# Kernel tuning notes

Measured on AMD Instinct MI355X. Metric: run time of the kernel, lower is better.

The kernel has to match this reference:

```python
import jax, jax.numpy as jnp
import numpy as np

D_MODEL = 1024
N_HEADS = 16
HEAD_DIM = 64
D_FF = 4096


def rmsnorm(x, w):
    eps = jnp.finfo(x.dtype).eps
    var = jnp.mean(jnp.square(x), axis=-1, keepdims=True)
    return x * jax.lax.rsqrt(var + eps) * w


def setup_inputs() -> dict:
    key = jax.random.key(0)
    ks = jax.random.split(key, 8)
    d, h, hd, dff = D_MODEL, N_HEADS, HEAD_DIM, D_FF
    s = 0.02
    return {
        "x": jax.random.normal(ks[0], (2, 2048, d), dtype=jnp.float32),
        "norm_w": jnp.ones((d,), dtype=jnp.float32),
        "Wq": jax.random.normal(ks[1], (d, h * hd), dtype=jnp.float32) * s,
        "Wk": jax.random.normal(ks[2], (d, h * hd), dtype=jnp.float32) * s,
        "Wv": jax.random.normal(ks[3], (d, h * hd), dtype=jnp.float32) * s,
        "Wo": jax.random.normal(ks[4], (h * hd, d), dtype=jnp.float32) * s,
        "W1": jax.random.normal(ks[5], (d, dff), dtype=jnp.float32) * s,
        "W2": jax.random.normal(ks[6], (dff, d), dtype=jnp.float32) * s,
    }


def reference(x, norm_w, Wq, Wk, Wv, Wo, W1, W2):
    B, T, d = x.shape
    h, hd = N_HEADS, HEAD_DIM
    scale = 1.0 / np.sqrt(hd)

    xn = rmsnorm(x, norm_w)

    # attention branch
    q = (xn @ Wq).reshape(B, T, h, hd).transpose(0, 2, 1, 3)  # [B,h,T,hd]
    k = (xn @ Wk).reshape(B, T, h, hd).transpose(0, 2, 1, 3)
    v = (xn @ Wv).reshape(B, T, h, hd).transpose(0, 2, 1, 3)
    attn = jnp.einsum("bhqd,bhkd->bhqk", q, k) * scale
    causal = jnp.tril(jnp.ones((T, T), dtype=bool))
    attn = jnp.where(causal, attn, -jnp.inf)
    attn = jax.nn.softmax(attn, axis=-1)
    out = jnp.einsum("bhqk,bhkd->bhqd", attn, v)
    out = out.transpose(0, 2, 1, 3).reshape(B, T, h * hd)
    attn_out = out @ Wo

    # FFN branch
    ffn_out = jax.nn.silu(xn @ W1) @ W2

    return x + attn_out + ffn_out
```

## Files before the change

kernel.cpp:

```cpp
#include <hip/hip_runtime.h>

#define DM   1024
#define DFF  4096
#define NH   16
#define HD   64
#define TT   2048
#define BT   4096
#define KC   5120

typedef unsigned short u16;
typedef unsigned int   u32;
typedef __attribute__((ext_vector_type(8))) short s16x8;
typedef __attribute__((ext_vector_type(4))) float f32x4;

__device__ __forceinline__ u16 f2bf(float f) {
  u32 u = __builtin_bit_cast(u32, f);
  u += 0x7fffu + ((u >> 16) & 1u);
  return (u16)(u >> 16);
}

__device__ __forceinline__ void gl2lds16(const void* g, void* l) {
  __builtin_amdgcn_global_load_lds((__attribute__((address_space(1))) void*)(g),
                                   (__attribute__((address_space(3))) void*)(l),
                                   16, 0, 0);
}

#define S_BARRIER() do { __builtin_amdgcn_s_barrier(); __builtin_amdgcn_sched_barrier(0); } while (0)
#define VMWAIT(n)   asm volatile("s_waitcnt vmcnt(" #n ")" ::: "memory")

__global__ __launch_bounds__(256) void rmsnorm_k(const float* __restrict__ x,
                                                 const float* __restrict__ w,
                                                 u16* __restrict__ xn) {
  const int row = blockIdx.x;
  const int t = threadIdx.x;
  const float4 v = ((const float4*)(x + (size_t)row * DM))[t];
  float ss = v.x*v.x + v.y*v.y + v.z*v.z + v.w*v.w;
  #pragma unroll
  for (int off = 32; off; off >>= 1) ss += __shfl_xor(ss, off, 64);
  __shared__ float red[4];
  if ((t & 63) == 0) red[t >> 6] = ss;
  __syncthreads();
  const float tot = red[0] + red[1] + red[2] + red[3];
  const float r = __builtin_amdgcn_rsqf(tot * (1.0f / DM) + 1.1920929e-7f);
  const float4 wv = ((const float4*)w)[t];
  u16* o = xn + (size_t)row * DM + t * 4;
  o[0] = f2bf(v.x * r * wv.x);
  o[1] = f2bf(v.y * r * wv.y);
  o[2] = f2bf(v.z * r * wv.z);
  o[3] = f2bf(v.w * r * wv.w);
}

__global__ __launch_bounds__(256) void wtrans_k(const float* __restrict__ W,
                                                u16* __restrict__ Wt,
                                                int K, int N, int pitch, int koff) {
  __shared__ float tile[32][33];
  const int n0 = blockIdx.x * 32, k0 = blockIdx.y * 32;
  const int tx = threadIdx.x, ty = threadIdx.y;
  #pragma unroll
  for (int i = 0; i < 4; ++i)
    tile[ty + i*8][tx] = W[(size_t)(k0 + ty + i*8) * N + n0 + tx];
  __syncthreads();
  #pragma unroll
  for (int i = 0; i < 4; ++i)
    Wt[(size_t)(n0 + ty + i*8) * pitch + koff + k0 + tx] = f2bf(tile[tx][ty + i*8]);
}

__global__ __launch_bounds__(256, 2) void gemm_fused(const u16* __restrict__ A,
                                                     const u16* __restrict__ Bt,
                                                     u16* __restrict__ qkb,
                                                     u16* __restrict__ vtg,
                                                     u16* __restrict__ acat) {
  const int K = 1024;
  __shared__ u16 sA[4 * 128 * 32];
  __shared__ u16 sB[4 * 128 * 32];
  const int t = threadIdx.x;
  const int lane = t & 63, wave = t >> 6;
  const int quad = lane >> 4, l4 = lane & 15;
  const int wy = wave >> 1, wx = wave & 1;
  const size_t mBase = (size_t)blockIdx.y * 128;
  const size_t nBase = (size_t)blockIdx.x * 128;
  const int r  = t >> 2;
  const int c8 = ((t & 3) ^ ((t >> 3) & 3)) * 8;
  const int qsw = (quad ^ ((l4 >> 1) & 3)) * 8;
  const u16* Ag0 = A + (mBase + r) * K + c8;
  const u16* Ag1 = Ag0 + (size_t)64 * K;
  const u16* Bg0 = Bt + (nBase + r) * K + c8;
  const u16* Bg1 = Bg0 + (size_t)64 * K;
  char* sAb = (char*)sA + (wave << 10);
  char* sBb = (char*)sB + (wave << 10);

  f32x4 acc[4][4];
  #pragma unroll
  for (int i = 0; i < 4; ++i)
    #pragma unroll
    for (int j = 0; j < 4; ++j)
      acc[i][j] = (f32x4)0.0f;

  auto issue = [&](int bf, int k0) {
    gl2lds16(Ag0 + k0, sAb + bf*8192);
    gl2lds16(Ag1 + k0, sAb + bf*8192 + 4096);
    gl2lds16(Bg0 + k0, sBb + bf*8192);
    gl2lds16(Bg1 + k0, sBb + bf*8192 + 4096);
  };

  auto compute = [&](int bf) {
    const u16* pA = sA + bf * 4096;
    const u16* pB = sB + bf * 4096;
    s16x8 af[4], bfr[4];
    #pragma unroll
    for (int i = 0; i < 4; ++i)
      af[i] = *(const s16x8*)&pA[(wy*64 + i*16 + l4) * 32 + qsw];
    #pragma unroll
    for (int j = 0; j < 4; ++j)
      bfr[j] = *(const s16x8*)&pB[(wx*64 + j*16 + l4) * 32 + qsw];
    #pragma unroll
    for (int i = 0; i < 4; ++i)
      #pragma unroll
      for (int j = 0; j < 4; ++j)
        acc[i][j] = __builtin_amdgcn_mfma_f32_16x16x32_bf16(af[i], bfr[j], acc[i][j], 0, 0, 0);
  };

  issue(0, 0); issue(1, 32); issue(2, 64);
  for (int kt = 0; kt < 30; ++kt) {
    VMWAIT(8);
    S_BARRIER();
    if (kt + 3 < 32) issue((kt + 3) & 3, (kt + 3) * 32);
    compute(kt & 3);
  }
  VMWAIT(4); S_BARRIER(); compute(30 & 3);
  VMWAIT(0); S_BARRIER(); compute(31 & 3);

  #pragma unroll
  for (int i = 0; i < 4; ++i) {
    const size_t row0 = mBase + wy*64 + i*16 + quad*4;
    #pragma unroll
    for (int j = 0; j < 4; ++j) {
      const int col = (int)nBase + wx*64 + j*16 + l4;
      if (nBase < 1024) {
        #pragma unroll
        for (int rg = 0; rg < 4; ++rg)
          qkb[(row0 + rg) * 2048 + col] = f2bf(acc[i][j][rg] * 0.18033688011f);
      } else if (nBase < 2048) {
        #pragma unroll
        for (int rg = 0; rg < 4; ++rg)
          qkb[(row0 + rg) * 2048 + col] = f2bf(acc[i][j][rg]);
      } else if (nBase < 3072) {
        const int cv = col - 2048, hh = cv >> 6, dd = cv & 63;
        const int bb = (int)(row0 >> 11), t0 = (int)(row0 & 2047);
        ushort4 pk;
        pk.x = f2bf(acc[i][j][0]); pk.y = f2bf(acc[i][j][1]);
        pk.z = f2bf(acc[i][j][2]); pk.w = f2bf(acc[i][j][3]);
        *(ushort4*)(vtg + ((size_t)((bb*16 + hh)*64 + dd)) * 2048 + t0) = pk;
      } else {
        #pragma unroll
        for (int rg = 0; rg < 4; ++rg) {
          float v = acc[i][j][rg];
          v = v / (1.0f + __expf(-v));
          acat[(row0 + rg) * (size_t)KC + 1024 + (col - 3072)] = f2bf(v);
        }
      }
    }
  }
}

__global__ __launch_bounds__(256, 2) void gemm_final(const u16* __restrict__ A,
                                                     const u16* __restrict__ Bt,
                                                     const float* __restrict__ x,
                                                     float* __restrict__ out) {
  __shared__ u16 sA[4 * 64 * 32];
  __shared__ u16 sB[4 * 128 * 32];
  const int t = threadIdx.x;
  const int lane = t & 63, wave = t >> 6;
  const int quad = lane >> 4, l4 = lane & 15;
  const int wy = wave >> 1, wx = wave & 1;
  const size_t mBase = (size_t)blockIdx.y * 64;
  const size_t nBase = (size_t)blockIdx.x * 128;
  const int r  = t >> 2;
  const int c8 = ((t & 3) ^ ((t >> 3) & 3)) * 8;
  const int qsw = (quad ^ ((l4 >> 1) & 3)) * 8;
  const u16* Ag  = A  + (mBase + r) * KC + c8;
  const u16* Bg0 = Bt + (nBase + r) * KC + c8;
  const u16* Bg1 = Bg0 + (size_t)64 * KC;
  char* sAb = (char*)sA + (wave << 10);
  char* sBb = (char*)sB + (wave << 10);

  f32x4 acc[2][4];
  #pragma unroll
  for (int i = 0; i < 2; ++i)
    #pragma unroll
    for (int j = 0; j < 4; ++j)
      acc[i][j] = (f32x4)0.0f;

  auto issue = [&](int bf, int k0) {
    gl2lds16(Ag  + k0, sAb + bf*4096);
    gl2lds16(Bg0 + k0, sBb + bf*8192);
    gl2lds16(Bg1 + k0, sBb + bf*8192 + 4096);
  };

  auto compute = [&](int bf) {
    const u16* pA = sA + bf * 2048;
    const u16* pB = sB + bf * 4096;
    s16x8 af[2], bfr[4];
    #pragma unroll
    for (int i = 0; i < 2; ++i)
      af[i] = *(const s16x8*)&pA[(wy*32 + i*16 + l4) * 32 + qsw];
    #pragma unroll
    for (int j = 0; j < 4; ++j)
      bfr[j] = *(const s16x8*)&pB[(wx*64 + j*16 + l4) * 32 + qsw];
    #pragma unroll
    for (int i = 0; i < 2; ++i)
      #pragma unroll
      for (int j = 0; j < 4; ++j)
        acc[i][j] = __builtin_amdgcn_mfma_f32_16x16x32_bf16(af[i], bfr[j], acc[i][j], 0, 0, 0);
  };

  const int NIT = KC / 32;
  issue(0, 0); issue(1, 32); issue(2, 64);
  for (int kt = 0; kt < NIT - 2; ++kt) {
    VMWAIT(6);
    S_BARRIER();
    if (kt + 3 < NIT) issue((kt + 3) & 3, (kt + 3) * 32);
    compute(kt & 3);
  }
  VMWAIT(3); S_BARRIER(); compute((NIT - 2) & 3);
  VMWAIT(0); S_BARRIER(); compute((NIT - 1) & 3);

  #pragma unroll
  for (int i = 0; i < 2; ++i) {
    const size_t row0 = mBase + wy*32 + i*16 + quad*4;
    #pragma unroll
    for (int j = 0; j < 4; ++j) {
      const int col = (int)nBase + wx*64 + j*16 + l4;
      #pragma unroll
      for (int rg = 0; rg < 4; ++rg) {
        const size_t idx = (row0 + rg) * (size_t)DM + col;
        out[idx] = x[idx] + acc[i][j][rg];
      }
    }
  }
}

__global__ __launch_bounds__(128) void attn_k(const u16* __restrict__ qk,
                                              const u16* __restrict__ vtg,
                                              u16* __restrict__ acat) {
  const int bh = blockIdx.x, b = bh >> 4, h = bh & 15;
  const int qt = 63 - blockIdx.y;
  const int qw = qt * 32;
  const int wave = threadIdx.x >> 6, lane = threadIdx.x & 63;
  const int quad = lane >> 4, l4 = lane & 15;
  const u16* Qp = qk + (size_t)b * TT * 2048 + h * HD;
  const u16* Kp = Qp + 1024;
  const u16* Vp = vtg + (size_t)bh * 64 * 2048;

  __shared__ u16 Pb[2][32][72];
  __shared__ float Ob[32][68];
  __shared__ float Lb[32];

  s16x8 qf[2][2];
  #pragma unroll
  for (int mi = 0; mi < 2; ++mi)
    #pragma unroll
    for (int kf = 0; kf < 2; ++kf)
      qf[mi][kf] = *(const s16x8*)(Qp + (size_t)(qw + mi*16 + l4) * 2048 + kf*32 + quad*8);

  const s16x8 ones = {0x3F80,0x3F80,0x3F80,0x3F80,0x3F80,0x3F80,0x3F80,0x3F80};

  f32x4 o[2][4];
  f32x4 lacc[2];
  #pragma unroll
  for (int mi = 0; mi < 2; ++mi) {
    lacc[mi] = (f32x4)0.0f;
    #pragma unroll
    for (int ni = 0; ni < 4; ++ni) o[mi][ni] = (f32x4)0.0f;
  }

  const int n   = (qt + 2) >> 1;
  const int n0  = (n + 1) >> 1;
  const int kt0 = wave ? n0 : 0;
  const int kt1 = wave ? n : n0;

  for (int kt = kt0; kt < kt1; ++kt) {
    const int k0 = kt * 64;

    f32x4 st[4][2];
    #pragma unroll
    for (int nj = 0; nj < 4; ++nj) {
      const u16* kr = Kp + (size_t)(k0 + nj*16 + l4) * 2048 + quad*8;
      const s16x8 kf0 = *(const s16x8*)kr;
      const s16x8 kf1 = *(const s16x8*)(kr + 32);
      #pragma unroll
      for (int mi = 0; mi < 2; ++mi) {
        f32x4 a = (f32x4)0.0f;
        a = __builtin_amdgcn_mfma_f32_16x16x32_bf16(kf0, qf[mi][0], a, 0, 0, 0);
        a = __builtin_amdgcn_mfma_f32_16x16x32_bf16(kf1, qf[mi][1], a, 0, 0, 0);
        st[nj][mi] = a;
      }
    }

    s16x8 vb[2][4];
    #pragma unroll
    for (int kf2 = 0; kf2 < 2; ++kf2)
      #pragma unroll
      for (int ni = 0; ni < 4; ++ni)
        vb[kf2][ni] = *(const s16x8*)(Vp + (size_t)(ni*16 + l4) * 2048 + k0 + kf2*32 + quad*8);

    if (k0 + 63 > qw) {
      #pragma unroll
      for (int nj = 0; nj < 4; ++nj)
        #pragma unroll
        for (int mi = 0; mi < 2; ++mi)
          #pragma unroll
          for (int rg = 0; rg < 4; ++rg) {
            const int key = k0 + nj*16 + quad*4 + rg;
            const int q   = qw + mi*16 + l4;
            if (key > q) st[nj][mi][rg] = -1e30f;
          }
    }

    #pragma unroll
    for (int nj = 0; nj < 4; ++nj)
      #pragma unroll
      for (int mi = 0; mi < 2; ++mi) {
        float p0 = __builtin_amdgcn_exp2f(st[nj][mi][0]);
        float p1 = __builtin_amdgcn_exp2f(st[nj][mi][1]);
        float p2 = __builtin_amdgcn_exp2f(st[nj][mi][2]);
        float p3 = __builtin_amdgcn_exp2f(st[nj][mi][3]);
        uint2 w;
        w.x = __builtin_amdgcn_perm(__builtin_bit_cast(u32, p1),
                                    __builtin_bit_cast(u32, p0), 0x07060302u);
        w.y = __builtin_amdgcn_perm(__builtin_bit_cast(u32, p3),
                                    __builtin_bit_cast(u32, p2), 0x07060302u);
        *(uint2*)&Pb[wave][mi*16 + l4][nj*16 + quad*4] = w;
      }

    #pragma unroll
    for (int kf2 = 0; kf2 < 2; ++kf2) {
      s16x8 pa[2];
      #pragma unroll
      for (int mi = 0; mi < 2; ++mi)
        pa[mi] = *(const s16x8*)&Pb[wave][mi*16 + l4][kf2*32 + quad*8];
      #pragma unroll
      for (int mi = 0; mi < 2; ++mi) {
        lacc[mi] = __builtin_amdgcn_mfma_f32_16x16x32_bf16(pa[mi], ones, lacc[mi], 0, 0, 0);
        #pragma unroll
        for (int ni = 0; ni < 4; ++ni)
          o[mi][ni] = __builtin_amdgcn_mfma_f32_16x16x32_bf16(pa[mi], vb[kf2][ni], o[mi][ni], 0, 0, 0);
      }
    }
  }

  if (wave == 1) {
    #pragma unroll
    for (int mi = 0; mi < 2; ++mi)
      #pragma unroll
      for (int rg = 0; rg < 4; ++rg) {
        const int row = mi*16 + quad*4 + rg;
        #pragma unroll
        for (int ni = 0; ni < 4; ++ni) Ob[row][ni*16 + l4] = o[mi][ni][rg];
        if (l4 == 0) Lb[row] = lacc[mi][rg];
      }
  }
  __syncthreads();
  if (wave == 0) {
    #pragma unroll
    for (int mi = 0; mi < 2; ++mi)
      #pragma unroll
      for (int rg = 0; rg < 4; ++rg) {
        const int row = mi*16 + quad*4 + rg;
        const float inv = 1.0f / (lacc[mi][rg] + Lb[row]);
        #pragma unroll
        for (int ni = 0; ni < 4; ++ni)
          Pb[0][row][ni*16 + l4] = f2bf((o[mi][ni][rg] + Ob[row][ni*16 + l4]) * inv);
      }
    #pragma unroll
    for (int it = 0; it < 4; ++it) {
      const int row = it*8 + (lane >> 3);
      const int c0  = (lane & 7) * 8;
      const s16x8 pk = *(const s16x8*)&Pb[0][row][c0];
      *(s16x8*)(acat + ((size_t)b * TT + qw + row) * KC + h*HD + c0) = pk;
    }
  }
}

extern "C" void kernel_launch(void* const* d_in, const int* in_sizes, int n_in,
                              void* d_out, int out_size, void* d_ws, size_t ws_size,
                              hipStream_t stream) {
  (void)in_sizes; (void)n_in; (void)out_size; (void)ws_size;
  const float* x  = (const float*)d_in[0];
  const float* nw = (const float*)d_in[1];
  const float* Wq = (const float*)d_in[2];
  const float* Wk = (const float*)d_in[3];
  const float* Wv = (const float*)d_in[4];
  const float* Wo = (const float*)d_in[5];
  const float* W1 = (const float*)d_in[6];
  const float* W2 = (const float*)d_in[7];

  char* ws = (char*)d_ws;
  u16*   xn      = (u16*)(ws);
  u16*   wqkv1_t = (u16*)(ws + ((size_t)8  << 20));
  u16*   bcat    = (u16*)(ws + ((size_t)22 << 20));
  u16*   qkb     = (u16*)(ws + ((size_t)32 << 20));
  u16*   vtg     = (u16*)(ws + ((size_t)48 << 20));
  u16*   acat    = (u16*)(ws + ((size_t)56 << 20));
  float* dout    = (float*)d_out;

  rmsnorm_k<<<BT, 256, 0, stream>>>(x, nw, xn);
  const dim3 tb(32, 8);
  wtrans_k<<<dim3(32, 32),  tb, 0, stream>>>(Wq, wqkv1_t,                      1024, 1024, 1024, 0);
  wtrans_k<<<dim3(32, 32),  tb, 0, stream>>>(Wk, wqkv1_t + (size_t)1024*1024,  1024, 1024, 1024, 0);
  wtrans_k<<<dim3(32, 32),  tb, 0, stream>>>(Wv, wqkv1_t + (size_t)2048*1024,  1024, 1024, 1024, 0);
  wtrans_k<<<dim3(128, 32), tb, 0, stream>>>(W1, wqkv1_t + (size_t)3072*1024,  1024, 4096, 1024, 0);
  wtrans_k<<<dim3(32, 32),  tb, 0, stream>>>(Wo, bcat,                         1024, 1024, 5120, 0);
  wtrans_k<<<dim3(32, 128), tb, 0, stream>>>(W2, bcat,                         4096, 1024, 5120, 1024);

  gemm_fused<<<dim3(56, 32), 256, 0, stream>>>(xn, wqkv1_t, qkb, vtg, acat);
  attn_k<<<dim3(32, 64), 128, 0, stream>>>(qkb, vtg, acat);
  gemm_final<<<dim3(8, 64), 256, 0, stream>>>(acat, bcat, x, dout);
}
```

Before: 372.5 us.

## Enlarge fused QKV/W1 GEMM tile to 256x256 with 8 waves and 2-deep prefetch

Grows the fused projection GEMM block tile from 128x128 to 256x256 and runs it with 512 threads (8 waves, 2x4 layout, each wave computing 128x64). The larger tile raises operand reuse per LDS load and cuts global traffic, and the pipeline is reorganized so loads are issued before compute with one barrier per step. MFMA sections are wrapped in s_setprio. The costs are twice the LDS per block (128 KB), higher register pressure from 32 accumulators, and only 448 blocks, which may hurt occupancy and wave balance across CUs.

Result: no change. 373.1 us (+0.2%).

```diff
diff --git a/kernel.cpp b/kernel.cpp
--- a/kernel.cpp
+++ b/kernel.cpp
@@ -65,74 +65,83 @@
     Wt[(size_t)(n0 + ty + i*8) * pitch + koff + k0 + tx] = f2bf(tile[tx][ty + i*8]);
 }
 
-__global__ __launch_bounds__(256, 2) void gemm_fused(const u16* __restrict__ A,
+__global__ __launch_bounds__(512, 2) void gemm_fused(const u16* __restrict__ A,
                                                      const u16* __restrict__ Bt,
                                                      u16* __restrict__ qkb,
                                                      u16* __restrict__ vtg,
                                                      u16* __restrict__ acat) {
   const int K = 1024;
-  __shared__ u16 sA[4 * 128 * 32];
-  __shared__ u16 sB[4 * 128 * 32];
+  __shared__ u16 sA[4 * 256 * 32];
+  __shared__ u16 sB[4 * 256 * 32];
   const int t = threadIdx.x;
   const int lane = t & 63, wave = t >> 6;
   const int quad = lane >> 4, l4 = lane & 15;
-  const int wy = wave >> 1, wx = wave & 1;
-  const size_t mBase = (size_t)blockIdx.y * 128;
-  const size_t nBase = (size_t)blockIdx.x * 128;
-  const int r  = t >> 2;
-  const int c8 = ((t & 3) ^ ((t >> 3) & 3)) * 8;
+  const int wy = wave >> 2, wx = wave & 3;
+  const size_t mBase = (size_t)blockIdx.y * 256;
+  const size_t nBase = (size_t)blockIdx.x * 256;
+
+  const int srow = lane >> 2;
+  const int scol = ((lane & 3) ^ ((lane >> 3) & 3)) * 8;
+  const u16* Ag0 = A  + (mBase + (size_t)(wave*2 + 0)*16 + srow) * K + scol;
+  const u16* Ag1 = A  + (mBase + (size_t)(wave*2 + 1)*16 + srow) * K + scol;
+  const u16* Bg0 = Bt + (nBase + (size_t)(wave*2 + 0)*16 + srow) * K + scol;
+  const u16* Bg1 = Bt + (nBase + (size_t)(wave*2 + 1)*16 + srow) * K + scol;
+  char* dA0 = (char*)sA + (wave*2 + 0) * 1024;
+  char* dA1 = (char*)sA + (wave*2 + 1) * 1024;
+  char* dB0 = (char*)sB + (wave*2 + 0) * 1024;
+  char* dB1 = (char*)sB + (wave*2 + 1) * 1024;
+
   const int qsw = (quad ^ ((l4 >> 1) & 3)) * 8;
-  const u16* Ag0 = A + (mBase + r) * K + c8;
-  const u16* Ag1 = Ag0 + (size_t)64 * K;
-  const u16* Bg0 = Bt + (nBase + r) * K + c8;
-  const u16* Bg1 = Bg0 + (size_t)64 * K;
-  char* sAb = (char*)sA + (wave << 10);
-  char* sBb = (char*)sB + (wave << 10);
-
-  f32x4 acc[4][4];
-  #pragma unroll
-  for (int i = 0; i < 4; ++i)
+
+  f32x4 acc[8][4];
+  #pragma unroll
+  for (int i = 0; i < 8; ++i)
     #pragma unroll
     for (int j = 0; j < 4; ++j)
       acc[i][j] = (f32x4)0.0f;
 
-  auto issue = [&](int bf, int k0) {
-    gl2lds16(Ag0 + k0, sAb + bf*8192);
-    gl2lds16(Ag1 + k0, sAb + bf*8192 + 4096);
-    gl2lds16(Bg0 + k0, sBb + bf*8192);
-    gl2lds16(Bg1 + k0, sBb + bf*8192 + 4096);
+  auto issue = [&](int slot, int k0) {
+    gl2lds16(Ag0 + k0, dA0 + slot*16384);
+    gl2lds16(Ag1 + k0, dA1 + slot*16384);
+    gl2lds16(Bg0 + k0, dB0 + slot*16384);
+    gl2lds16(Bg1 + k0, dB1 + slot*16384);
   };
 
-  auto compute = [&](int bf) {
-    const u16* pA = sA + bf * 4096;
-    const u16* pB = sB + bf * 4096;
-    s16x8 af[4], bfr[4];
-    #pragma unroll
-    for (int i = 0; i < 4; ++i)
-      af[i] = *(const s16x8*)&pA[(wy*64 + i*16 + l4) * 32 + qsw];
-    #pragma unroll
-    for (int j = 0; j < 4; ++j)
-      bfr[j] = *(const s16x8*)&pB[(wx*64 + j*16 + l4) * 32 + qsw];
-    #pragma unroll
-    for (int i = 0; i < 4; ++i)
-      #pragma unroll
-      for (int j = 0; j < 4; ++j)
-        acc[i][j] = __builtin_amdgcn_mfma_f32_16x16x32_bf16(af[i], bfr[j], acc[i][j], 0, 0, 0);
+  auto compute = [&](int slot) {
+    const u16* pA = sA + slot * 8192;
+    const u16* pB = sB + slot * 8192;
+    s16x8 bfr[4];
+    #pragma unroll
+    for (int nj = 0; nj < 4; ++nj)
+      bfr[nj] = *(const s16x8*)&pB[(wx*64 + nj*16 + l4) * 32 + qsw];
+    __builtin_amdgcn_s_setprio(1);
+    #pragma unroll
+    for (int mi = 0; mi < 8; ++mi) {
+      const s16x8 af = *(const s16x8*)&pA[(wy*128 + mi*16 + l4) * 32 + qsw];
+      #pragma unroll
+      for (int nj = 0; nj < 4; ++nj)
+        acc[mi][nj] = __builtin_amdgcn_mfma_f32_16x16x32_bf16(af, bfr[nj], acc[mi][nj], 0, 0, 0);
+    }
+    __builtin_amdgcn_s_setprio(0);
   };
 
-  issue(0, 0); issue(1, 32); issue(2, 64);
-  for (int kt = 0; kt < 30; ++kt) {
-    VMWAIT(8);
+  const int NT = K / 32;
+  issue(0, 0); issue(1, 32);
+  VMWAIT(4);
+  S_BARRIER();
+  for (int kt = 0; kt < NT - 2; ++kt) {
+    issue((kt + 2) & 3, (kt + 2) * 32);
+    compute(kt & 3);
+    VMWAIT(4);
     S_BARRIER();
-    if (kt + 3 < 32) issue((kt + 3) & 3, (kt + 3) * 32);
-    compute(kt & 3);
-  }
-  VMWAIT(4); S_BARRIER(); compute(30 & 3);
-  VMWAIT(0); S_BARRIER(); compute(31 & 3);
-
-  #pragma unroll
-  for (int i = 0; i < 4; ++i) {
-    const size_t row0 = mBase + wy*64 + i*16 + quad*4;
+  }
+  compute((NT - 2) & 3);
+  VMWAIT(0); S_BARRIER();
+  compute((NT - 1) & 3);
+
+  #pragma unroll
+  for (int i = 0; i < 8; ++i) {
+    const size_t row0 = mBase + wy*128 + i*16 + quad*4;
     #pragma unroll
     for (int j = 0; j < 4; ++j) {
       const int col = (int)nBase + wx*64 + j*16 + l4;
@@ -413,7 +422,7 @@
   wtrans_k<<<dim3(32, 32),  tb, 0, stream>>>(Wo, bcat,                         1024, 1024, 5120, 0);
   wtrans_k<<<dim3(32, 128), tb, 0, stream>>>(W2, bcat,                         4096, 1024, 5120, 1024);
 
-  gemm_fused<<<dim3(56, 32), 256, 0, stream>>>(xn, wqkv1_t, qkb, vtg, acat);
+  gemm_fused<<<dim3(28, 16), 512, 0, stream>>>(xn, wqkv1_t, qkb, vtg, acat);
   attn_k<<<dim3(32, 64), 128, 0, stream>>>(qkb, vtg, acat);
   gemm_final<<<dim3(8, 64), 256, 0, stream>>>(acat, bcat, x, dout);
 }
```
